# Performance work log

Hardware: AMD Instinct MI355X
Metric: run time of the kernel (lower is better)

The kernel has to match this reference:

```python
import jax, jax.numpy as jnp
import numpy as np

N = 200000   # residue nodes
E = 800000   # backbone edges
P = 500000   # contact pairs to score
DIN = 128    # in_channels['res']
H = 256      # hidden per layer
L = 3        # layers


def _sage(x, src, dst, Wl, Wr, b):
    # SAGEConv: mean-aggregate source-neighbor features into dst, plus root transform
    msum = jax.ops.segment_sum(x[src], dst, num_segments=N)
    deg = jax.ops.segment_sum(jnp.ones((src.shape[0],), x.dtype), dst, num_segments=N)
    m = msum / jnp.maximum(deg, 1.0)[:, None]
    return m @ Wl + x @ Wr + b


def _graphnorm(x, w, b, ms, eps=1e-5):
    # PyG GraphNorm over a single graph (batch of all zeros)
    mu = x.mean(axis=0)
    out = x - ms * mu
    var = (out * out).mean(axis=0)
    return out / jnp.sqrt(var + eps) * w + b


def setup_inputs() -> dict:
    key = jax.random.key(0)
    ks = jax.random.split(key, 40)
    s = 0.05
    inp = {
        'x_res': jax.random.normal(ks[0], (N, DIN), jnp.float32),
        'edge_index': jax.random.randint(ks[1], (2, E), 0, N),
        'contact_pred_index': jax.random.randint(ks[2], (2, P), 0, N),
    }
    dims = [DIN, H, H]
    j = 3
    for i in range(L):
        inp['Wl%d' % i] = jax.random.normal(ks[j], (dims[i], H), jnp.float32) * s; j += 1
        inp['Wr%d' % i] = jax.random.normal(ks[j], (dims[i], H), jnp.float32) * s; j += 1
        inp['bc%d' % i] = jnp.zeros((H,), jnp.float32)
        inp['gnw%d' % i] = jnp.ones((H,), jnp.float32)
        inp['gnb%d' % i] = jnp.zeros((H,), jnp.float32)
        inp['gns%d' % i] = jnp.ones((H,), jnp.float32)
    inp['dyt_alpha'] = jnp.float32(0.5)
    inp['dyt_w'] = jnp.ones((H * L,), jnp.float32)
    inp['dyt_b'] = jnp.zeros((H * L,), jnp.float32)
    XD = [512, 512]
    inp['W1'] = jax.random.normal(ks[j], (H * L, XD[0]), jnp.float32) * s; j += 1
    inp['b1'] = jnp.zeros((XD[0],), jnp.float32)
    inp['W2'] = jax.random.normal(ks[j], (XD[0], XD[1]), jnp.float32) * s; j += 1
    inp['b2'] = jnp.zeros((XD[1],), jnp.float32)
    inp['W3'] = jax.random.normal(ks[j], (XD[1], DIN), jnp.float32) * s; j += 1
    inp['b3'] = jnp.zeros((DIN,), jnp.float32)
    CD = [256, 128]
    inp['C1'] = jax.random.normal(ks[j], (2 * DIN, CD[0]), jnp.float32) * s; j += 1
    inp['c1'] = jnp.zeros((CD[0],), jnp.float32)
    inp['C2'] = jax.random.normal(ks[j], (CD[0], CD[1]), jnp.float32) * s; j += 1
    inp['c2'] = jnp.zeros((CD[1],), jnp.float32)
    inp['C3'] = jax.random.normal(ks[j], (CD[1], 1), jnp.float32) * s; j += 1
    inp['c3'] = jnp.zeros((1,), jnp.float32)
    return inp


def reference(x_res, edge_index, contact_pred_index,
              Wl0, Wr0, bc0, gnw0, gnb0, gns0,
              Wl1, Wr1, bc1, gnw1, gnb1, gns1,
              Wl2, Wr2, bc2, gnw2, gnb2, gns2,
              dyt_alpha, dyt_w, dyt_b,
              W1, b1, W2, b2, W3, b3,
              C1, c1, C2, c2, C3, c3):
    gelu = lambda v: jax.nn.gelu(v, approximate=False)
    src, dst = edge_index[0], edge_index[1]
    inz = x_res
    h = x_res
    layers = [(Wl0, Wr0, bc0, gnw0, gnb0, gns0),
              (Wl1, Wr1, bc1, gnw1, gnb1, gns1),
              (Wl2, Wr2, bc2, gnw2, gnb2, gns2)]
    outs = []
    for i, (Wl, Wr, b, gw, gb, gs) in enumerate(layers):
        prev = h
        h = gelu(_sage(h, src, dst, Wl, Wr, b))
        h = _graphnorm(h, gw, gb, gs)
        if i > 0:
            h = h + prev
        outs.append(h)
    z = jnp.concatenate(outs, axis=1)                 # JumpingKnowledge 'cat' -> [N, 3H]
    z = jnp.tanh(dyt_alpha * z) * dyt_w + dyt_b       # DynamicTanh
    z = gelu(z @ W1 + b1)
    z = gelu(z @ W2 + b2)
    z = z @ W3 + b3
    z = z + inz                                       # residual back to input features
    z = z / (jnp.linalg.norm(z, axis=1, keepdims=True) + 1e-10)
    pair = jnp.concatenate([z[contact_pred_index[0]], z[contact_pred_index[1]]], axis=1)
    e = gelu(pair @ C1 + c1)
    e = gelu(e @ C2 + c2)
    scores = (e @ C3 + c3)[:, 0]
    return jax.nn.sigmoid(scores)
```

## Files before the change

### kernel.cpp

```cpp
#include <hip/hip_runtime.h>
#include <math.h>

typedef unsigned short u16;
typedef __attribute__((ext_vector_type(8))) short short8v;
typedef __attribute__((ext_vector_type(4))) float f32x4;

__device__ __forceinline__ float geluf(float x) {
    return 0.5f * x * (1.0f + erff(x * 0.70710678118654752f));
}
__device__ __forceinline__ float bf2f(u16 u) { return __uint_as_float((unsigned)u << 16); }
__device__ __forceinline__ u16 f2bf(float f) {
    unsigned x = __float_as_uint(f);
    unsigned r = x + 0x7FFFu + ((x >> 16) & 1u);
    return (u16)(r >> 16);
}
__device__ __forceinline__ float tanhfast(float x) {
    float cx = fminf(fmaxf(x, -15.f), 15.f);
    float t = __expf(2.f * cx);
    return (t - 1.f) / (t + 1.f);
}

template<bool BF>
__device__ __forceinline__ float4 ld4(const void* base, long long elemOff) {
    if (BF) {
        ushort4 u = *(const ushort4*)((const u16*)base + elemOff);
        return make_float4(bf2f(u.x), bf2f(u.y), bf2f(u.z), bf2f(u.w));
    } else {
        return *(const float4*)((const float*)base + elemOff);
    }
}

__global__ __launch_bounds__(256) void cnt_kernel(const int* __restrict__ dst, int* __restrict__ cnt, int E, int Nn) {
    int e = blockIdx.x * 256 + threadIdx.x;
    if (e < E) {
        int d = dst[e];
        if ((unsigned)d < (unsigned)Nn) atomicAdd(&cnt[d], 1);
    }
}
__global__ __launch_bounds__(256) void scan1_kernel(const int* __restrict__ cnt, int* __restrict__ rp,
                                                    int* __restrict__ bs, int n) {
    __shared__ int sh[256];
    int i = blockIdx.x * 256 + threadIdx.x;
    int v = (i < n) ? cnt[i] : 0;
    sh[threadIdx.x] = v; __syncthreads();
    for (int o = 1; o < 256; o <<= 1) {
        int t = (threadIdx.x >= o) ? sh[threadIdx.x - o] : 0;
        __syncthreads();
        sh[threadIdx.x] += t;
        __syncthreads();
    }
    if (i < n) rp[i] = sh[threadIdx.x] - v;
    if (threadIdx.x == 255) bs[blockIdx.x] = sh[255];
}
__global__ __launch_bounds__(1024) void scan2_kernel(int* __restrict__ bs, int nb) {
    __shared__ int sh[1024];
    int v = (threadIdx.x < nb) ? bs[threadIdx.x] : 0;
    sh[threadIdx.x] = v; __syncthreads();
    for (int o = 1; o < 1024; o <<= 1) {
        int t = (threadIdx.x >= o) ? sh[threadIdx.x - o] : 0;
        __syncthreads();
        sh[threadIdx.x] += t;
        __syncthreads();
    }
    if (threadIdx.x < nb) bs[threadIdx.x] = sh[threadIdx.x] - v;
}
__global__ __launch_bounds__(256) void scan3_kernel(int* __restrict__ rp, int* __restrict__ cur,
                                                    const int* __restrict__ bs, int n, int E) {
    int i = blockIdx.x * 256 + threadIdx.x;
    if (i < n) {
        int v = rp[i] + bs[blockIdx.x];
        rp[i] = v;
        cur[i] = v;
    }
    if (i == 0) rp[n] = E;
}
__global__ __launch_bounds__(256) void fill_kernel(const int* __restrict__ src, const int* __restrict__ dst,
                                                   int* __restrict__ cur, int* __restrict__ srcs, int E, int Nn) {
    int e = blockIdx.x * 256 + threadIdx.x;
    if (e >= E) return;
    int d = dst[e];
    if ((unsigned)d >= (unsigned)Nn) return;
    int s = src[e];
    if ((unsigned)s >= (unsigned)Nn) s = 0;
    int p = atomicAdd(&cur[d], 1);
    srcs[p] = s;
}

template<bool L0>
__global__ __launch_bounds__(256) void agg_csr_kernel(const void* __restrict__ X, int ldx,
    const int* __restrict__ rp, const int* __restrict__ srcs,
    u16* __restrict__ m, int c0, int rows)
{
    int lrow = blockIdx.x * 4 + (threadIdx.x >> 6);
    if (lrow >= rows) return;
    int lane = threadIdx.x & 63;
    int r = c0 + lrow;
    int b = rp[r], e = rp[r + 1];
    float inv = 1.0f / fmaxf((float)(e - b), 1.0f);
    if (L0) {
        float a0 = 0.f, a1 = 0.f, c0a = 0.f, c1a = 0.f;
        int i = b;
        for (; i + 2 <= e; i += 2) {
            int s0 = srcs[i], s1 = srcs[i + 1];
            float2 v0 = *(const float2*)((const float*)X + (long long)s0 * ldx + lane * 2);
            float2 v1 = *(const float2*)((const float*)X + (long long)s1 * ldx + lane * 2);
            a0 += v0.x; a1 += v0.y;
            c0a += v1.x; c1a += v1.y;
        }
        if (i < e) {
            int s0 = srcs[i];
            float2 v0 = *(const float2*)((const float*)X + (long long)s0 * ldx + lane * 2);
            a0 += v0.x; a1 += v0.y;
        }
        a0 += c0a; a1 += c1a;
        ushort2 o; o.x = f2bf(a0 * inv); o.y = f2bf(a1 * inv);
        *(ushort2*)(m + (long long)lrow * 128 + lane * 2) = o;
    } else {
        float a0 = 0.f, a1 = 0.f, a2 = 0.f, a3 = 0.f;
        float b0 = 0.f, b1 = 0.f, b2 = 0.f, b3 = 0.f;
        int i = b;
        for (; i + 2 <= e; i += 2) {
            int s0 = srcs[i], s1 = srcs[i + 1];
            ushort4 u0 = *(const ushort4*)((const u16*)X + (long long)s0 * ldx + lane * 4);
            ushort4 u1 = *(const ushort4*)((const u16*)X + (long long)s1 * ldx + lane * 4);
            a0 += bf2f(u0.x); a1 += bf2f(u0.y); a2 += bf2f(u0.z); a3 += bf2f(u0.w);
            b0 += bf2f(u1.x); b1 += bf2f(u1.y); b2 += bf2f(u1.z); b3 += bf2f(u1.w);
        }
        if (i < e) {
            int s0 = srcs[i];
            ushort4 u0 = *(const ushort4*)((const u16*)X + (long long)s0 * ldx + lane * 4);
            a0 += bf2f(u0.x); a1 += bf2f(u0.y); a2 += bf2f(u0.z); a3 += bf2f(u0.w);
        }
        a0 += b0; a1 += b1; a2 += b2; a3 += b3;
        ushort4 o;
        o.x = f2bf(a0 * inv); o.y = f2bf(a1 * inv); o.z = f2bf(a2 * inv); o.w = f2bf(a3 * inv);
        *(ushort4*)(m + (long long)lrow * 256 + lane * 4) = o;
    }
}

struct PrepArgs {
    const float* W[11];
    short* outp[11];
    int K[11], Nc[11], kOff[11], Ktot[11];
    int start[12];
};
__global__ __launch_bounds__(256) void prep_all_kernel(PrepArgs a) {
    int idx = blockIdx.x * 256 + threadIdx.x;
    if (idx >= a.start[11]) return;
    int si = 0;
    #pragma unroll
    for (int j = 1; j < 11; ++j) si += (idx >= a.start[j]);
    int local = idx - a.start[si];
    int Nc = a.Nc[si];
    int k = local / Nc, n = local % Nc;
    a.outp[si][(long long)n * a.Ktot[si] + a.kOff[si] + k] = (short)f2bf(a.W[si][local]);
}

template<bool BF>
__device__ __forceinline__ void loadrow(const void* base, long long off, short8v& o0, short8v& o1) {
    if (BF) {
        const short* p = (const short*)base + off;
        o0 = *(const short8v*)p;
        o1 = *(const short8v*)(p + 8);
    } else {
        const float* p = (const float*)base + off;
        float4 a = *(const float4*)p;
        float4 b = *(const float4*)(p + 4);
        float4 c = *(const float4*)(p + 8);
        float4 d = *(const float4*)(p + 12);
        short8v r0, r1;
        r0[0] = (short)f2bf(a.x); r0[1] = (short)f2bf(a.y); r0[2] = (short)f2bf(a.z); r0[3] = (short)f2bf(a.w);
        r0[4] = (short)f2bf(b.x); r0[5] = (short)f2bf(b.y); r0[6] = (short)f2bf(b.z); r0[7] = (short)f2bf(b.w);
        r1[0] = (short)f2bf(c.x); r1[1] = (short)f2bf(c.y); r1[2] = (short)f2bf(c.z); r1[3] = (short)f2bf(c.w);
        r1[4] = (short)f2bf(d.x); r1[5] = (short)f2bf(d.y); r1[6] = (short)f2bf(d.z); r1[7] = (short)f2bf(d.w);
        o0 = r0; o1 = r1;
    }
}

template<int EPI, bool A1BF, bool A2BF, bool CBF, bool STAT, bool NORM>
__global__ __launch_bounds__(256) void mm_kernel(
    const void* __restrict__ A1, int lda1,
    const void* __restrict__ A2, int lda2,
    int K1, int K2,
    const short* __restrict__ Bhi, int ldb,
    const float* __restrict__ bias,
    const float* __restrict__ resid, int ldres,
    float* __restrict__ s1, float* __restrict__ s2,
    void* __restrict__ C, int ldc, int M)
{
    __shared__ short As[128 * 40];
    __shared__ short Bh[128 * 40];
    __shared__ float cst[256];
    __shared__ float rsq[128][2];
    const int t = threadIdx.x;
    const int rowbase = blockIdx.y * 128;
    const int colbase = blockIdx.x * 128;
    const int srow = t >> 1;
    const int sh = (t & 1) << 4;
    const int lane = t & 63;
    const int wv = t >> 6;
    const int wr = (wv >> 1) << 6;
    const int wc = (wv & 1) << 6;
    const int l15 = lane & 15;
    const int kreg = (lane >> 4) << 3;
    const int rgrp = (lane >> 4) << 2;
    if (STAT && t < 256) cst[t] = 0.f;
    f32x4 acc[4][4] = {};
    const int k1t = K1 >> 5;
    const int KT = (K1 + K2) >> 5;

    for (int kt = 0; kt < KT; ++kt) {
        const bool p1 = kt < k1t;
        {
            short8v a0 = {0,0,0,0,0,0,0,0}, a1 = {0,0,0,0,0,0,0,0};
            int r = rowbase + srow;
            if (r < M) {
                const int kbl = (p1 ? kt : kt - k1t) << 5;
                if (p1) loadrow<A1BF>(A1, (long long)r * lda1 + kbl + sh, a0, a1);
                else    loadrow<A2BF>(A2, (long long)r * lda2 + kbl + sh, a0, a1);
            }
            *(short8v*)&As[srow * 40 + sh]     = a0;
            *(short8v*)&As[srow * 40 + sh + 8] = a1;
        }
        {
            long long boff = (long long)(colbase + srow) * ldb + (kt << 5) + sh;
            *(short8v*)&Bh[srow * 40 + sh]     = *(const short8v*)(Bhi + boff);
            *(short8v*)&Bh[srow * 40 + sh + 8] = *(const short8v*)(Bhi + boff + 8);
        }
        __syncthreads();
        short8v a4[4], b4[4];
        #pragma unroll
        for (int mr = 0; mr < 4; ++mr)
            a4[mr] = *(short8v*)&As[(wr + mr * 16 + l15) * 40 + kreg];
        #pragma unroll
        for (int nr = 0; nr < 4; ++nr)
            b4[nr] = *(short8v*)&Bh[(wc + nr * 16 + l15) * 40 + kreg];
        #pragma unroll
        for (int mr = 0; mr < 4; ++mr)
            #pragma unroll
            for (int nr = 0; nr < 4; ++nr)
                acc[mr][nr] = __builtin_amdgcn_mfma_f32_16x16x32_bf16(a4[mr], b4[nr], acc[mr][nr], 0, 0, 0);
        __syncthreads();
    }

    if (NORM) {
        float rs[4][4] = {};
        #pragma unroll
        for (int nr = 0; nr < 4; ++nr) {
            int c = colbase + wc + nr * 16 + l15;
            float bi = bias[c];
            #pragma unroll
            for (int mr = 0; mr < 4; ++mr)
                #pragma unroll
                for (int i = 0; i < 4; ++i) {
                    int r = rowbase + wr + mr * 16 + rgrp + i;
                    float v = 0.f;
                    if (r < M) {
                        v = acc[mr][nr][i] + bi;
                        if (EPI == 3) v += resid[(long long)r * ldres + c];
                        if (EPI == 1) v = geluf(v);
                    }
                    acc[mr][nr][i] = v;
                    rs[mr][i] += v * v;
                }
        }
        #pragma unroll
        for (int mr = 0; mr < 4; ++mr)
            #pragma unroll
            for (int i = 0; i < 4; ++i) {
                float s = rs[mr][i];
                s += __shfl_xor(s, 1); s += __shfl_xor(s, 2);
                s += __shfl_xor(s, 4); s += __shfl_xor(s, 8);
                rs[mr][i] = s;
            }
    if (l15 == 0) {
            #pragma unroll
            for (int mr = 0; mr < 4; ++mr)
                #pragma unroll
                for (int i = 0; i < 4; ++i)
                    rsq[wr + mr * 16 + rgrp + i][wv & 1] = rs[mr][i];
        }
        __syncthreads();
        #pragma unroll
        for (int mr = 0; mr < 4; ++mr)
            #pragma unroll
            for (int i = 0; i < 4; ++i) {
                int rl = wr + mr * 16 + rgrp + i;
                int r = rowbase + rl;
                if (r >= M) continue;
                float inv = 1.0f / (sqrtf(rsq[rl][0] + rsq[rl][1]) + 1e-10f);
                #pragma unroll
                for (int nr = 0; nr < 4; ++nr) {
                    int c = colbase + wc + nr * 16 + l15;
                    float v = acc[mr][nr][i] * inv;
                    if (CBF) ((u16*)C)[(long long)r * ldc + c] = f2bf(v);
                    else     ((float*)C)[(long long)r * ldc + c] = v;
                }
            }
    } else {
        #pragma unroll
        for (int nr = 0; nr < 4; ++nr) {
            int c = colbase + wc + nr * 16 + l15;
            float bi = bias[c];
            float cp = 0.f, cq = 0.f;
            #pragma unroll
            for (int mr = 0; mr < 4; ++mr)
                #pragma unroll
                for (int i = 0; i < 4; ++i) {
                    int r = rowbase + wr + mr * 16 + rgrp + i;
                    if (r >= M) continue;
                    float v = acc[mr][nr][i] + bi;
                    if (EPI == 1) v = geluf(v);
                    if (EPI == 3) v += resid[(long long)r * ldres + c];
                    if (CBF) ((u16*)C)[(long long)r * ldc + c] = f2bf(v);
                    else     ((float*)C)[(long long)r * ldc + c] = v;
                    if (STAT) { cp += v; cq += v * v; }
                }
            if (STAT) {
                cp += __shfl_xor(cp, 16); cp += __shfl_xor(cp, 32);
                cq += __shfl_xor(cq, 16); cq += __shfl_xor(cq, 32);
                if (lane < 16) {
                    int cl = wc + nr * 16 + l15;
                    atomicAdd(&cst[cl], cp);
                    atomicAdd(&cst[128 + cl], cq);
                }
            }
        }
        if (STAT) {
            __syncthreads();
            if (t < 128) {
                atomicAdd(s1 + colbase + t, cst[t]);
                atomicAdd(s2 + colbase + t, cst[128 + t]);
            }
        }
    }
}

__global__ __launch_bounds__(256) void pair_kernel(
    const u16* __restrict__ zf, const int* __restrict__ g1, const int* __restrict__ g2,
    int Nn, int P,
    const short* __restrict__ C1t, const float* __restrict__ c1,
    const short* __restrict__ C2t, const float* __restrict__ c2,
    const float* __restrict__ C3, const float* __restrict__ c3,
    float* __restrict__ out)
{
    __shared__ short E1s[128 * 264];
    __shared__ float sc[128][2];
    const int t = threadIdx.x;
    const int lane = t & 63;
    const int wv = t >> 6;
    const int wr = (wv >> 1) << 6;
    const int wc = (wv & 1) << 6;
    const int l15 = lane & 15;
    const int kreg = (lane >> 4) << 3;
    const int rgrp = (lane >> 4) << 2;
    const int p0 = blockIdx.x * 128;

    int gidx[2][4];
    #pragma unroll
    for (int mr = 0; mr < 4; ++mr) {
        int pr = p0 + wr + mr * 16 + l15;
        int a = (pr < P) ? g1[pr] : 0;
        if ((unsigned)a >= (unsigned)Nn) a = 0;
        gidx[0][mr] = a;
        int b = (pr < P) ? g2[pr] : 0;
        if ((unsigned)b >= (unsigned)Nn) b = 0;
        gidx[1][mr] = b;
    }

    #pragma unroll
    for (int ch = 0; ch < 2; ++ch) {
        f32x4 acc[4][4] = {};
        #pragma unroll
        for (int kt = 0; kt < 8; ++kt) {
            const int half = kt >> 2;
            const int kl = ((kt & 3) << 5) + kreg;
            short8v a4[4], b4[4];
            #pragma unroll
            for (int mr = 0; mr < 4; ++mr)
                a4[mr] = *(const short8v*)((const short*)zf + (long long)gidx[half][mr] * 128 + kl);
            #pragma unroll
            for (int nr = 0; nr < 4; ++nr)
                b4[nr] = *(const short8v*)(C1t + (long long)(ch * 128 + wc + nr * 16 + l15) * 256 + (kt << 5) + kreg);
            #pragma unroll
            for (int mr = 0; mr < 4; ++mr)
                #pragma unroll
                for (int nr = 0; nr < 4; ++nr)
                    acc[mr][nr] = __builtin_amdgcn_mfma_f32_16x16x32_bf16(a4[mr], b4[nr], acc[mr][nr], 0, 0, 0);
        }
        #pragma unroll
        for (int nr = 0; nr < 4; ++nr) {
            int cc = wc + nr * 16 + l15;
            float bi = c1[ch * 128 + cc];
            #pragma unroll
            for (int mr = 0; mr < 4; ++mr)
                #pragma unroll
                for (int i = 0; i < 4; ++i) {
                    float v = geluf(acc[mr][nr][i] + bi);
                    E1s[(wr + mr * 16 + rgrp + i) * 264 + ch * 128 + cc] = (short)f2bf(v);
                }
        }
    }
    __syncthreads();

    f32x4 acc[4][4] = {};
    #pragma unroll
    for (int kt = 0; kt < 8; ++kt) {
        short8v a4[4], b4[4];
        #pragma unroll
        for (int mr = 0; mr < 4; ++mr)
            a4[mr] = *(short8v*)&E1s[(wr + mr * 16 + l15) * 264 + (kt << 5) + kreg];
        #pragma unroll
        for (int nr = 0; nr < 4; ++nr)
            b4[nr] = *(const short8v*)(C2t + (long long)(wc + nr * 16 + l15) * 256 + (kt << 5) + kreg);
        #pragma unroll
        for (int mr = 0; mr < 4; ++mr)
            #pragma unroll
            for (int nr = 0; nr < 4; ++nr)
                acc[mr][nr] = __builtin_amdgcn_mfma_f32_16x16x32_bf16(a4[mr], b4[nr], acc[mr][nr], 0, 0, 0);
    }

    float pr_[4][4] = {};
    #pragma unroll
    for (int nr = 0; nr < 4; ++nr) {
        int cc = wc + nr * 16 + l15;
        float bi = c2[cc];
        float w3 = C3[cc];
        #pragma unroll
        for (int mr = 0; mr < 4; ++mr)
            #pragma unroll
            for (int i = 0; i < 4; ++i)
                pr_[mr][i] += geluf(acc[mr][nr][i] + bi) * w3;
    }
    #pragma unroll
    for (int mr = 0; mr < 4; ++mr)
        #pragma unroll
        for (int i = 0; i < 4; ++i) {
            float s = pr_[mr][i];
            s += __shfl_xor(s, 1); s += __shfl_xor(s, 2);
            s += __shfl_xor(s, 4); s += __shfl_xor(s, 8);
            pr_[mr][i] = s;
        }
    if (l15 == 0) {
        #pragma unroll
        for (int mr = 0; mr < 4; ++mr)
            #pragma unroll
            for (int i = 0; i < 4; ++i)
                sc[wr + mr * 16 + rgrp + i][wv & 1] = pr_[mr][i];
    }
    __syncthreads();
    if (t < 128) {
        int p = p0 + t;
        if (p < P) {
            float x = sc[t][0] + sc[t][1] + c3[0];
            out[p] = 1.0f / (1.0f + expf(-x));
        }
    }
}

template<bool DYT>
__global__ __launch_bounds__(256) void gn_apply_kernel(u16* __restrict__ G, int ldg,
    const u16* __restrict__ prev, int ldp, int M,
    const float* __restrict__ s1, const float* __restrict__ s2,
    const float* __restrict__ gw, const float* __restrict__ gb, const float* __restrict__ gs,
    float invN,
    const float* __restrict__ dA, const float* __restrict__ dW, const float* __restrict__ dB)
{
    long long idx = (long long)blockIdx.x * blockDim.x + threadIdx.x;
    if (idx >= (long long)M * 64) return;
    int c0 = (int)(idx & 63) << 2;
    long long r = idx >> 6;
    float4 g = ld4<true>(G, r * ldg + c0);
    float o[4] = {g.x, g.y, g.z, g.w};
    float alpha = DYT ? dA[0] : 0.f;
    #pragma unroll
    for (int j = 0; j < 4; ++j) {
        int c = c0 + j;
        float mu = s1[c] * invN;
        float ms = gs[c];
        float var = s2[c] * invN - mu * mu * ms * (2.0f - ms);
        float rstd = rsqrtf(var + 1e-5f);
        o[j] = (o[j] - ms * mu) * rstd * gw[c] + gb[c];
    }
    if (prev) {
        float4 pv = ld4<true>(prev, r * ldp + c0);
        o[0] += pv.x; o[1] += pv.y; o[2] += pv.z; o[3] += pv.w;
    }
    if (DYT) {
        #pragma unroll
        for (int j = 0; j < 4; ++j)
            o[j] = tanhfast(alpha * o[j]) * dW[c0 + j] + dB[c0 + j];
    }
    ushort4 u; u.x = f2bf(o[0]); u.y = f2bf(o[1]); u.z = f2bf(o[2]); u.w = f2bf(o[3]);
    *(ushort4*)((u16*)G + r * ldg + c0) = u;
}

__global__ __launch_bounds__(256) void dyt512_kernel(u16* __restrict__ Z,
    const float* __restrict__ alphaP, const float* __restrict__ w, const float* __restrict__ b,
    long long total)
{
    long long idx = (long long)blockIdx.x * blockDim.x + threadIdx.x;
    if (idx >= total) return;
    int c0 = (int)(idx & 63) << 3;
    long long r = idx >> 6;
    float alpha = alphaP[0];
    short8v z = *(short8v*)(Z + r * 768 + c0);
    float4 w0 = *(const float4*)(w + c0);
    float4 w1 = *(const float4*)(w + c0 + 4);
    float4 b0 = *(const float4*)(b + c0);
    float4 b1 = *(const float4*)(b + c0 + 4);
    short8v o;
    o[0] = (short)f2bf(tanhfast(alpha * bf2f((u16)z[0])) * w0.x + b0.x);
    o[1] = (short)f2bf(tanhfast(alpha * bf2f((u16)z[1])) * w0.y + b0.y);
    o[2] = (short)f2bf(tanhfast(alpha * bf2f((u16)z[2])) * w0.z + b0.z);
    o[3] = (short)f2bf(tanhfast(alpha * bf2f((u16)z[3])) * w0.w + b0.w);
    o[4] = (short)f2bf(tanhfast(alpha * bf2f((u16)z[4])) * w1.x + b1.x);
    o[5] = (short)f2bf(tanhfast(alpha * bf2f((u16)z[5])) * w1.y + b1.y);
    o[6] = (short)f2bf(tanhfast(alpha * bf2f((u16)z[6])) * w1.z + b1.z);
    o[7] = (short)f2bf(tanhfast(alpha * bf2f((u16)z[7])) * w1.w + b1.w);
    *(short8v*)(Z + r * 768 + c0) = o;
}

extern "C" void kernel_launch(void* const* d_in, const int* in_sizes, int n_in,
                              void* d_out, int out_size, void* d_ws, size_t ws_size,
                              hipStream_t stream) {
    const float* x_res = (const float*)d_in[0];
    const int* eidx = (const int*)d_in[1];
    const int* cidx = (const int*)d_in[2];
    const int N = in_sizes[0] / 128;
    const int E = in_sizes[1] / 2;
    const int P = in_sizes[2] / 2;
    const int* src = eidx;
    const int* dst = eidx + E;
    const int* g1 = cidx;
    const int* g2 = cidx + P;
    const float* Wl[3] = {(const float*)d_in[3], (const float*)d_in[9],  (const float*)d_in[15]};
    const float* Wr[3] = {(const float*)d_in[4], (const float*)d_in[10], (const float*)d_in[16]};
    const float* bc[3] = {(const float*)d_in[5], (const float*)d_in[11], (const float*)d_in[17]};
    const float* gnw[3] = {(const float*)d_in[6], (const float*)d_in[12], (const float*)d_in[18]};
    const float* gnb[3] = {(const float*)d_in[7], (const float*)d_in[13], (const float*)d_in[19]};
    const float* gns[3] = {(const float*)d_in[8], (const float*)d_in[14], (const float*)d_in[20]};
    const float* alphaP = (const float*)d_in[21];
    const float* dytw = (const float*)d_in[22];
    const float* dytb = (const float*)d_in[23];
    const float* W1 = (const float*)d_in[24]; const float* b1 = (const float*)d_in[25];
    const float* W2 = (const float*)d_in[26]; const float* b2 = (const float*)d_in[27];
    const float* W3 = (const float*)d_in[28]; const float* b3 = (const float*)d_in[29];
    const float* C1 = (const float*)d_in[30]; const float* c1 = (const float*)d_in[31];
    const float* C2 = (const float*)d_in[32]; const float* c2 = (const float*)d_in[33];
    const float* C3 = (const float*)d_in[34]; const float* c3 = (const float*)d_in[35];
    float* out = (float*)d_out;

    char* ws = (char*)d_ws;
    size_t off = 0;
    size_t zOff  = off; off += (size_t)N * 768 * 2;     off = (off + 255) & ~(size_t)255;
    size_t stOff = off; off += 2048;                    off = (off + 255) & ~(size_t)255;
    size_t zfOff = off; off += (size_t)N * 128 * 2;     off = (off + 255) & ~(size_t)255;
    size_t rpOff = off; off += (size_t)(N + 1) * 4;     off = (off + 255) & ~(size_t)255;
    size_t curOff = off; off += (size_t)N * 4;          off = (off + 255) & ~(size_t)255;
    size_t srcsOff = off; off += (size_t)E * 4;         off = (off + 255) & ~(size_t)255;
    size_t bsOff = off; off += 4096;                    off = (off + 255) & ~(size_t)255;
    static const size_t se[8] = {65536, 131072, 131072, 393216, 262144, 65536, 65536, 32768};
    short* wt[8];
    for (int i = 0; i < 8; ++i) {
        wt[i] = (short*)(ws + off);
        off += 2 * se[i];
        off = (off + 255) & ~(size_t)255;
    }
    size_t pOff = off;
    size_t avail = ws_size > pOff ? ws_size - pOff : 0;

    u16*   Z    = (u16*)(ws + zOff);
    float* st   = (float*)(ws + stOff);
    u16*   zf   = (u16*)(ws + zfOff);
    int*   rp   = (int*)(ws + rpOff);
    int*   cur  = (int*)(ws + curOff);
    int*   srcs = (int*)(ws + srcsOff);
    int*   bs   = (int*)(ws + bsOff);
    u16*   pbuf = (u16*)(ws + pOff);

    int NC = (int)((avail /  512) & ~(size_t)127); if (NC < 128) NC = 128; if (NC > N) NC = N;
    int S  = (int)((avail / 2048) & ~(size_t)127); if (S  < 128) S  = 128; if (S  > N) S  = N;

    dim3 blk(256);

    {
        PrepArgs a;
        const float* Ws[11] = {Wl[0], Wr[0], Wl[1], Wr[1], Wl[2], Wr[2], W1, W2, W3, C1, C2};
        short* Os[11] = {wt[0], wt[0], wt[1], wt[1], wt[2], wt[2], wt[3], wt[4], wt[5], wt[6], wt[7]};
        int Ks[11]    = {128, 128, 256, 256, 256, 256, 768, 512, 512, 256, 256};
        int Ncs[11]   = {256, 256, 256, 256, 256, 256, 512, 512, 128, 256, 128};
        int kOffs[11] = {0, 128, 0, 256, 0, 256, 0, 0, 0, 0, 0};
        int Ktots[11] = {256, 256, 512, 512, 512, 512, 768, 512, 512, 256, 256};
        int s = 0;
        for (int i = 0; i < 11; ++i) {
            a.W[i] = Ws[i]; a.outp[i] = Os[i];
            a.K[i] = Ks[i]; a.Nc[i] = Ncs[i]; a.kOff[i] = kOffs[i]; a.Ktot[i] = Ktots[i];
            a.start[i] = s;
            s += Ks[i] * Ncs[i];
        }
        a.start[11] = s;
        prep_all_kernel<<<(s + 255) / 256, 256, 0, stream>>>(a);
    }

    int nb = (N + 255) / 256;
    hipMemsetAsync(cur, 0, (size_t)N * 4, stream);
    cnt_kernel<<<(E + 255) / 256, 256, 0, stream>>>(dst, cur, E, N);
    scan1_kernel<<<nb, 256, 0, stream>>>(cur, rp, bs, N);
    scan2_kernel<<<1, 1024, 0, stream>>>(bs, nb);
    scan3_kernel<<<nb, 256, 0, stream>>>(rp, cur, bs, N, E);
    fill_kernel<<<(E + 255) / 256, 256, 0, stream>>>(src, dst, cur, srcs, E, N);

    u16* m = pbuf;
    for (int l = 0; l < 3; ++l) {
        u16* Zl = Z + l * 256;
        hipMemsetAsync(st, 0, 512 * 4, stream);
        for (int c0 = 0; c0 < N; c0 += NC) {
            int rows = (N - c0 < NC) ? (N - c0) : NC;
            int aggblocks = (rows + 3) / 4;
            dim3 grid(2, (rows + 127) / 128);
            if (l == 0) {
                agg_csr_kernel<true><<<aggblocks, 256, 0, stream>>>(x_res, 128, rp, srcs, m, c0, rows);
                mm_kernel<1, true, false, true, true, false><<<grid, blk, 0, stream>>>(
                    m, 128, x_res + (size_t)c0 * 128, 128, 128, 128,
                    wt[0], 256, bc[0], nullptr, 0, st, st + 256,
                    Zl + (size_t)c0 * 768, 768, rows);
            } else {
                const u16* h = Z + (l - 1) * 256;
                agg_csr_kernel<false><<<aggblocks, 256, 0, stream>>>(h, 768, rp, srcs, m, c0, rows);
                mm_kernel<1, true, true, true, true, false><<<grid, blk, 0, stream>>>(
                    m, 256, h + (size_t)c0 * 768, 768, 256, 256,
                    wt[l], 512, bc[l], nullptr, 0, st, st + 256,
                    Zl + (size_t)c0 * 768, 768, rows);
            }
        }
        const u16* prev = (l == 0) ? nullptr : (Z + (l - 1) * 256);
        int gnblocks = (int)(((long long)N * 64 + 255) / 256);
        if (l == 2)
            gn_apply_kernel<true><<<gnblocks, 256, 0, stream>>>(
                Zl, 768, prev, 768, N, st, st + 256, gnw[l], gnb[l], gns[l], 1.0f / (float)N,
                alphaP, dytw + 512, dytb + 512);
        else
            gn_apply_kernel<false><<<gnblocks, 256, 0, stream>>>(
                Zl, 768, prev, 768, N, st, st + 256, gnw[l], gnb[l], gns[l], 1.0f / (float)N,
                nullptr, nullptr, nullptr);
    }

    dyt512_kernel<<<(int)(((long long)N * 64 + 255) / 256), 256, 0, stream>>>(
        Z, alphaP, dytw, dytb, (long long)N * 64);

    {
        short* t1c = (short*)pbuf;
        short* t2c = t1c + (size_t)S * 512;
        for (int r0 = 0; r0 < N; r0 += S) {
            int rows = (N - r0 < S) ? (N - r0) : S;
            mm_kernel<1, true, true, true, false, false><<<dim3(4, (rows + 127) / 128), blk, 0, stream>>>(
                Z + (size_t)r0 * 768, 768, nullptr, 0, 768, 0,
                wt[3], 768, b1, nullptr, 0, nullptr, nullptr, t1c, 512, rows);
            mm_kernel<1, true, true, true, false, false><<<dim3(4, (rows + 127) / 128), blk, 0, stream>>>(
                t1c, 512, nullptr, 0, 512, 0,
                wt[4], 512, b2, nullptr, 0, nullptr, nullptr, t2c, 512, rows);
            mm_kernel<3, true, true, true, false, true><<<dim3(1, (rows + 127) / 128), blk, 0, stream>>>(
                t2c, 512, nullptr, 0, 512, 0,
                wt[5], 512, b3, x_res + (size_t)r0 * 128, 128, nullptr, nullptr,
                zf + (size_t)r0 * 128, 128, rows);
        }
    }

    pair_kernel<<<(P + 127) / 128, blk, 0, stream>>>(
        zf, g1, g2, N, P, wt[6], c1, wt[7], c2, C3, c3, out);
}
```

Baseline: 3.569 ms.

## Precompute per-node C1 projections and gather-add them in pair scoring

Splits the first pair-MLP layer algebraically: concat(z[a],z[b])@C1 equals z[a]@C1_top + z[b]@C1_bot. Two per-node GEMMs over N rows produce U and V, which reuse the Z buffer. The pair kernel then only gathers the U and V rows, adds them, applies GELU and runs the second layer. This replaces the K=256 GEMM over P pairs with a K=128 GEMM over N nodes plus elementwise work. The pair kernel now uses 64-row tiles and stages C2 through LDS each k-step, which adds per-step barriers and stores U/V in bf16, a small extra rounding.

Result: faster. 3.398 ms (-4.8%).

```diff
diff --git a/kernel.cpp b/kernel.cpp
--- a/kernel.cpp
+++ b/kernel.cpp
@@ -273,7 +273,7 @@
                 s += __shfl_xor(s, 4); s += __shfl_xor(s, 8);
                 rs[mr][i] = s;
             }
-    if (l15 == 0) {
+        if (l15 == 0) {
             #pragma unroll
             for (int mr = 0; mr < 4; ++mr)
                 #pragma unroll
@@ -337,103 +337,84 @@
 }
 
 __global__ __launch_bounds__(256) void pair_kernel(
-    const u16* __restrict__ zf, const int* __restrict__ g1, const int* __restrict__ g2,
+    const u16* __restrict__ U, const u16* __restrict__ V,
+    const int* __restrict__ g1, const int* __restrict__ g2,
     int Nn, int P,
-    const short* __restrict__ C1t, const float* __restrict__ c1,
     const short* __restrict__ C2t, const float* __restrict__ c2,
     const float* __restrict__ C3, const float* __restrict__ c3,
     float* __restrict__ out)
 {
-    __shared__ short E1s[128 * 264];
-    __shared__ float sc[128][2];
+    __shared__ short E1s[64 * 264];
+    __shared__ short Bs[128 * 40];
+    __shared__ float sc[64][2];
     const int t = threadIdx.x;
     const int lane = t & 63;
     const int wv = t >> 6;
-    const int wr = (wv >> 1) << 6;
+    const int wr = (wv >> 1) << 5;
     const int wc = (wv & 1) << 6;
     const int l15 = lane & 15;
     const int kreg = (lane >> 4) << 3;
     const int rgrp = (lane >> 4) << 2;
-    const int p0 = blockIdx.x * 128;
-
-    int gidx[2][4];
-    #pragma unroll
-    for (int mr = 0; mr < 4; ++mr) {
-        int pr = p0 + wr + mr * 16 + l15;
-        int a = (pr < P) ? g1[pr] : 0;
-        if ((unsigned)a >= (unsigned)Nn) a = 0;
-        gidx[0][mr] = a;
-        int b = (pr < P) ? g2[pr] : 0;
-        if ((unsigned)b >= (unsigned)Nn) b = 0;
-        gidx[1][mr] = b;
-    }
-
-    #pragma unroll
-    for (int ch = 0; ch < 2; ++ch) {
-        f32x4 acc[4][4] = {};
-        #pragma unroll
-        for (int kt = 0; kt < 8; ++kt) {
-            const int half = kt >> 2;
-            const int kl = ((kt & 3) << 5) + kreg;
-            short8v a4[4], b4[4];
-            #pragma unroll
-            for (int mr = 0; mr < 4; ++mr)
-                a4[mr] = *(const short8v*)((const short*)zf + (long long)gidx[half][mr] * 128 + kl);
-            #pragma unroll
-            for (int nr = 0; nr < 4; ++nr)
-                b4[nr] = *(const short8v*)(C1t + (long long)(ch * 128 + wc + nr * 16 + l15) * 256 + (kt << 5) + kreg);
-            #pragma unroll
-            for (int mr = 0; mr < 4; ++mr)
-                #pragma unroll
-                for (int nr = 0; nr < 4; ++nr)
-                    acc[mr][nr] = __builtin_amdgcn_mfma_f32_16x16x32_bf16(a4[mr], b4[nr], acc[mr][nr], 0, 0, 0);
-        }
-        #pragma unroll
-        for (int nr = 0; nr < 4; ++nr) {
-            int cc = wc + nr * 16 + l15;
-            float bi = c1[ch * 128 + cc];
-            #pragma unroll
-            for (int mr = 0; mr < 4; ++mr)
-                #pragma unroll
-                for (int i = 0; i < 4; ++i) {
-                    float v = geluf(acc[mr][nr][i] + bi);
-                    E1s[(wr + mr * 16 + rgrp + i) * 264 + ch * 128 + cc] = (short)f2bf(v);
-                }
+    const int p0 = blockIdx.x * 64;
+
+    {
+        int p = t >> 2, q = t & 3;
+        int pr = p0 + p;
+        int a = (pr < P) ? g1[pr] : 0;  if ((unsigned)a >= (unsigned)Nn) a = 0;
+        int b = (pr < P) ? g2[pr] : 0;  if ((unsigned)b >= (unsigned)Nn) b = 0;
+        const u16* up = U + (long long)a * 256 + q * 64;
+        const u16* vp = V + (long long)b * 256 + q * 64;
+        short* ep = &E1s[p * 264 + q * 64];
+        #pragma unroll
+        for (int j = 0; j < 8; ++j) {
+            short8v uu = *(const short8v*)(up + j * 8);
+            short8v vv = *(const short8v*)(vp + j * 8);
+            short8v oo;
+            #pragma unroll
+            for (int x = 0; x < 8; ++x)
+                oo[x] = (short)f2bf(geluf(bf2f((u16)uu[x]) + bf2f((u16)vv[x])));
+            *(short8v*)(ep + j * 8) = oo;
         }
     }
     __syncthreads();
 
-    f32x4 acc[4][4] = {};
-    #pragma unroll
+    f32x4 acc[2][4] = {};
+    const int srow = t >> 1;
+    const int sh2 = (t & 1) << 4;
     for (int kt = 0; kt < 8; ++kt) {
-        short8v a4[4], b4[4];
-        #pragma unroll
-        for (int mr = 0; mr < 4; ++mr)
+        long long boff = (long long)srow * 256 + (kt << 5) + sh2;
+        *(short8v*)&Bs[srow * 40 + sh2]     = *(const short8v*)(C2t + boff);
+        *(short8v*)&Bs[srow * 40 + sh2 + 8] = *(const short8v*)(C2t + boff + 8);
+        __syncthreads();
+        short8v a4[2], b4[4];
+        #pragma unroll
+        for (int mr = 0; mr < 2; ++mr)
             a4[mr] = *(short8v*)&E1s[(wr + mr * 16 + l15) * 264 + (kt << 5) + kreg];
         #pragma unroll
         for (int nr = 0; nr < 4; ++nr)
-            b4[nr] = *(const short8v*)(C2t + (long long)(wc + nr * 16 + l15) * 256 + (kt << 5) + kreg);
-        #pragma unroll
-        for (int mr = 0; mr < 4; ++mr)
+            b4[nr] = *(short8v*)&Bs[(wc + nr * 16 + l15) * 40 + kreg];
+        #pragma unroll
+        for (int mr = 0; mr < 2; ++mr)
             #pragma unroll
             for (int nr = 0; nr < 4; ++nr)
                 acc[mr][nr] = __builtin_amdgcn_mfma_f32_16x16x32_bf16(a4[mr], b4[nr], acc[mr][nr], 0, 0, 0);
-    }
-
-    float pr_[4][4] = {};
+        __syncthreads();
+    }
+
+    float pr_[2][4] = {};
     #pragma unroll
     for (int nr = 0; nr < 4; ++nr) {
         int cc = wc + nr * 16 + l15;
         float bi = c2[cc];
         float w3 = C3[cc];
         #pragma unroll
-        for (int mr = 0; mr < 4; ++mr)
+        for (int mr = 0; mr < 2; ++mr)
             #pragma unroll
             for (int i = 0; i < 4; ++i)
                 pr_[mr][i] += geluf(acc[mr][nr][i] + bi) * w3;
     }
     #pragma unroll
-    for (int mr = 0; mr < 4; ++mr)
+    for (int mr = 0; mr < 2; ++mr)
         #pragma unroll
         for (int i = 0; i < 4; ++i) {
             float s = pr_[mr][i];
@@ -443,13 +424,13 @@
         }
     if (l15 == 0) {
         #pragma unroll
-        for (int mr = 0; mr < 4; ++mr)
+        for (int mr = 0; mr < 2; ++mr)
             #pragma unroll
             for (int i = 0; i < 4; ++i)
                 sc[wr + mr * 16 + rgrp + i][wv & 1] = pr_[mr][i];
     }
     __syncthreads();
-    if (t < 128) {
+    if (t < 64) {
         int p = p0 + t;
         if (p < P) {
             float x = sc[t][0] + sc[t][1] + c3[0];
@@ -554,7 +535,7 @@
     char* ws = (char*)d_ws;
     size_t off = 0;
     size_t zOff  = off; off += (size_t)N * 768 * 2;     off = (off + 255) & ~(size_t)255;
-    size_t stOff = off; off += 2048;                    off = (off + 255) & ~(size_t)255;
+    size_t stOff = off; off += 4096;                    off = (off + 255) & ~(size_t)255;
     size_t zfOff = off; off += (size_t)N * 128 * 2;     off = (off + 255) & ~(size_t)255;
     size_t rpOff = off; off += (size_t)(N + 1) * 4;     off = (off + 255) & ~(size_t)255;
     size_t curOff = off; off += (size_t)N * 4;          off = (off + 255) & ~(size_t)255;
@@ -572,6 +553,7 @@
 
     u16*   Z    = (u16*)(ws + zOff);
     float* st   = (float*)(ws + stOff);
+    float* zb   = (float*)(ws + stOff + 2048);
     u16*   zf   = (u16*)(ws + zfOff);
     int*   rp   = (int*)(ws + rpOff);
     int*   cur  = (int*)(ws + curOff);
@@ -602,6 +584,7 @@
         a.start[11] = s;
         prep_all_kernel<<<(s + 255) / 256, 256, 0, stream>>>(a);
     }
+    hipMemsetAsync(zb, 0, 1024, stream);
 
     int nb = (N + 255) / 256;
     hipMemsetAsync(cur, 0, (size_t)N * 4, stream);
@@ -667,6 +650,15 @@
         }
     }
 
-    pair_kernel<<<(P + 127) / 128, blk, 0, stream>>>(
-        zf, g1, g2, N, P, wt[6], c1, wt[7], c2, C3, c3, out);
-}
+    u16* U = Z;
+    u16* V = Z + (size_t)N * 256;
+    mm_kernel<0, true, true, true, false, false><<<dim3(2, (N + 127) / 128), blk, 0, stream>>>(
+        zf, 128, nullptr, 0, 128, 0,
+        wt[6], 256, c1, nullptr, 0, nullptr, nullptr, U, 256, N);
+    mm_kernel<0, true, true, true, false, false><<<dim3(2, (N + 127) / 128), blk, 0, stream>>>(
+        zf, 128, nullptr, 0, 128, 0,
+        wt[6] + 128, 256, zb, nullptr, 0, nullptr, nullptr, V, 256, N);
+
+    pair_kernel<<<(P + 63) / 64, blk, 0, stream>>>(
+        U, V, g1, g2, N, P, wt[7], c2, C3, c3, out);
+}
```
